# Performance work log

Hardware: AMD Instinct MI355X
Metric: run time of the kernel (lower is better)

The kernel has to match this reference:

```python
import jax, jax.numpy as jnp
import numpy as np

B, T, C, H = 4, 2048, 1024, 16
HD = C // H  # head dim = 64


def setup_inputs() -> dict:
    key = jax.random.key(0)
    k1, k2, k3, k4, k5 = jax.random.split(key, 5)
    s_in = 1.0 / np.sqrt(C)
    return {
        "x": jax.random.normal(k1, (B, T, C), dtype=jnp.float32),
        "W_attn": jax.random.uniform(k2, (C, 3 * C), dtype=jnp.float32, minval=-s_in, maxval=s_in),
        "b_attn": jax.random.uniform(k3, (3 * C,), dtype=jnp.float32, minval=-s_in, maxval=s_in),
        "W_proj": jax.random.uniform(k4, (C, C), dtype=jnp.float32, minval=-s_in, maxval=s_in),
        "b_proj": jax.random.uniform(k5, (C,), dtype=jnp.float32, minval=-s_in, maxval=s_in),
    }


def reference(x, W_attn, b_attn, W_proj, b_proj):
    Bx, Tx, Cx = x.shape
    qkv = x @ W_attn + b_attn                      # [B,T,3C]
    q, k, v = jnp.split(qkv, 3, axis=2)
    # [B,T,C] -> [B,H,T,HD]
    def heads(t):
        return t.reshape(Bx, Tx, H, HD).transpose(0, 2, 1, 3)
    q, k, v = heads(q), heads(k), heads(v)
    scale = 1.0 / np.sqrt(HD).astype(np.float32)
    att = jnp.einsum('bhqd,bhkd->bhqk', q, k) * scale
    causal = jnp.tril(jnp.ones((Tx, Tx), dtype=bool))
    att = jnp.where(causal[None, None], att, -jnp.inf)
    att = jax.nn.softmax(att, axis=-1)
    y = jnp.einsum('bhqk,bhkd->bhqd', att, v)      # [B,H,T,HD]
    y = y.transpose(0, 2, 1, 3).reshape(Bx, Tx, Cx)
    return y @ W_proj + b_proj
```

## Files before the change

### kernel.cpp

```cpp
#include <hip/hip_runtime.h>
#include <math.h>

#define Bn 4
#define Tn 2048
#define Cn 1024
#define Hn 16
#define HDn 64
#define Mn (Bn * Tn)

typedef unsigned short u16;
typedef unsigned int u32;
typedef __attribute__((ext_vector_type(8))) short bf16x8;
typedef __attribute__((ext_vector_type(8))) unsigned short us8;
typedef __attribute__((ext_vector_type(4))) float f32x4;
typedef __attribute__((ext_vector_type(16))) float f32x16;
typedef __attribute__((ext_vector_type(4))) unsigned int u32x4;

__device__ __forceinline__ float b2f(u16 u) {
    return __uint_as_float(((u32)u) << 16);
}
__device__ __forceinline__ u16 f2b(float f) {
    u32 u = __float_as_uint(f);
    return (u16)((u + 0x7FFFu + ((u >> 16) & 1u)) >> 16);
}
__device__ __forceinline__ u32 cvtpk(float a, float b) {
    u32 d;
    asm("v_cvt_pk_bf16_f32 %0, %1, %2" : "=v"(d) : "v"(a), "v"(b));
    return d;
}
__device__ __forceinline__ void pswap(u32& a, u32& b) {
    asm("v_permlane32_swap_b32 %0, %1" : "+v"(a), "+v"(b));
}

__device__ __forceinline__ int xcd_work(int bid, int nwg) {
    return (bid & 7) * (nwg >> 3) + (bid >> 3);
}

#define GLL(srcp, dstp)                                                     \
    __builtin_amdgcn_global_load_lds(                                       \
        (const __attribute__((address_space(1))) u32*)(srcp),               \
        (__attribute__((address_space(3))) u32*)(dstp), 16, 0, 0)

__global__ __launch_bounds__(256) void cvt_f32_bf16_kernel(
    const float4* __restrict__ in, ushort4* __restrict__ out, int n4)
{
    int i = blockIdx.x * 256 + threadIdx.x;
    if (i < n4) {
        float4 v = in[i];
        ushort4 o;
        o.x = f2b(v.x); o.y = f2b(v.y); o.z = f2b(v.z); o.w = f2b(v.w);
        out[i] = o;
    }
}

__global__ __launch_bounds__(256) void transpose_cvt_kernel(
    const float* __restrict__ in, u16* __restrict__ out, int R, int Cc)
{
    __shared__ u16 t[32][33];
    const int c0 = blockIdx.x * 32, r0 = blockIdx.y * 32;
    const int tx = threadIdx.x & 31, ty = threadIdx.x >> 5;
    #pragma unroll
    for (int i = 0; i < 32; i += 8)
        t[ty + i][tx] = f2b(in[(size_t)(r0 + ty + i) * Cc + c0 + tx]);
    __syncthreads();
    #pragma unroll
    for (int i = 0; i < 32; i += 8)
        out[(size_t)(c0 + ty + i) * R + r0 + tx] = t[tx][ty + i];
}

template <bool OUT_BF16, bool QKV_MODE>
__global__ __launch_bounds__(256) void gemm_bf16_kernel(
    const u16* __restrict__ A, const u16* __restrict__ BT,
    const float* __restrict__ bias,
    u16* __restrict__ outb, float* __restrict__ outf, u16* __restrict__ vTout,
    int N, int K, int nx)
{
    __shared__ u16 Al[128 * 32];
    __shared__ u16 Bl[128 * 32];

    const int tid = threadIdx.x;
    const int workid = xcd_work(blockIdx.x, gridDim.x);
    const int brow = (workid / nx) * 128;
    const int bcol = (workid % nx) * 128;
    const int w  = tid >> 6;
    const int wr = w >> 1, wc = w & 1;
    const int l  = tid & 63;
    const int lr = l & 15;
    const int lk = (l >> 4) << 3;

    f32x4 acc[4][4];
    #pragma unroll
    for (int m = 0; m < 4; ++m)
        #pragma unroll
        for (int n = 0; n < 4; ++n) acc[m][n] = (f32x4){0.f, 0.f, 0.f, 0.f};

    for (int k0 = 0; k0 < K; k0 += 32) {
        __syncthreads();
        #pragma unroll
        for (int i = 0; i < 2; ++i) {
            const int c   = i * 256 + tid;
            const int row = c >> 2;
            const int col = (c & 3) << 3;
            GLL(&A [(size_t)(brow + row) * K + k0 + col],
                &Al[(size_t)(i * 256 + (tid & 192)) * 8]);
            GLL(&BT[(size_t)(bcol + row) * K + k0 + col],
                &Bl[(size_t)(i * 256 + (tid & 192)) * 8]);
        }
        __syncthreads();

        bf16x8 a[4], b[4];
        #pragma unroll
        for (int m = 0; m < 4; ++m)
            a[m] = *(const bf16x8*)&Al[(wr * 64 + m * 16 + lr) * 32 + lk];
        #pragma unroll
        for (int n = 0; n < 4; ++n)
            b[n] = *(const bf16x8*)&Bl[(wc * 64 + n * 16 + lr) * 32 + lk];

        __builtin_amdgcn_s_setprio(1);
        #pragma unroll
        for (int m = 0; m < 4; ++m)
            #pragma unroll
            for (int n = 0; n < 4; ++n)
                acc[m][n] = __builtin_amdgcn_mfma_f32_16x16x32_bf16(
                    a[m], b[n], acc[m][n], 0, 0, 0);
        __builtin_amdgcn_s_setprio(0);
    }

    const int orow0 = brow + wr * 64 + ((l >> 4) << 2);
    const int ocol0 = bcol + wc * 64 + lr;
    if (QKV_MODE && bcol >= 2048) {
        #pragma unroll
        for (int n = 0; n < 4; ++n) {
            const int c = ocol0 + n * 16 - 2048;
            const float bv = bias[ocol0 + n * 16];
            #pragma unroll
            for (int m = 0; m < 4; ++m) {
                const int row0 = orow0 + m * 16;
                const int bb = row0 >> 11, t0 = row0 & 2047;
                ushort4 pk;
                pk.x = f2b(acc[m][n][0] + bv);
                pk.y = f2b(acc[m][n][1] + bv);
                pk.z = f2b(acc[m][n][2] + bv);
                pk.w = f2b(acc[m][n][3] + bv);
                *(ushort4*)&vTout[((size_t)bb * Cn + c) * Tn + t0] = pk;
            }
        }
    } else {
        #pragma unroll
        for (int n = 0; n < 4; ++n) {
            const int col = ocol0 + n * 16;
            const float bv = bias[col];
            #pragma unroll
            for (int m = 0; m < 4; ++m) {
                #pragma unroll
                for (int r = 0; r < 4; ++r) {
                    const int row = orow0 + m * 16 + r;
                    const float v = acc[m][n][r] + bv;
                    if (OUT_BF16) outb[(size_t)row * N + col] = f2b(v);
                    else          outf[(size_t)row * N + col] = v;
                }
            }
        }
    }
}

__global__ __launch_bounds__(256, 2) void attn_mfma6_kernel(
    const u16* __restrict__ qkvb, const u16* __restrict__ vT,
    u16* __restrict__ yb)
{
    __shared__ u16 Kb[2][64 * 64];
    __shared__ u16 Vb[2][64 * 64];

    const int tid = threadIdx.x;
    const int w   = tid >> 6;
    const int l   = tid & 63;
    const int q31 = l & 31;
    const int hi  = l >> 5;
    const int work = xcd_work(blockIdx.x, 512);
    const int pr  = work & 7;
    const int bh  = work >> 3;
    const int b   = bh >> 4, h = bh & 15;

    const float S2 = 0.18033688f;

    const u16* Kg = qkvb + (size_t)(b * Tn) * (3 * Cn) + Cn + h * HDn;
    const u16* Vg = vT + (size_t)bh * HDn * Tn;

    const int srow = l >> 3;
    const int schk = ((l & 7) ^ srow) << 3;
    const int rloc = w * 16;
    const int rsw8 = q31 & 7;

    #pragma unroll 1
    for (int half = 0; half < 2; ++half) {
        const int qt = half ? (15 - pr) : pr;
        const int ktmax = 2 * qt + 2;
        const int qrow0 = qt * 128 + w * 32;
        const int qglob = qrow0 + q31;

        const u16* Qp = qkvb + (size_t)(b * Tn + qglob) * (3 * Cn)
                        + h * HDn + hi * 8;
        bf16x8 qf[4];
        #pragma unroll
        for (int c = 0; c < 4; ++c) qf[c] = *(const bf16x8*)(Qp + c * 16);

        f32x16 O0, O1;
        #pragma unroll
        for (int r = 0; r < 16; ++r) { O0[r] = 0.f; O1[r] = 0.f; }
        float m = -INFINITY, ls = 0.f;

        #pragma unroll
        for (int jc = 0; jc < 2; ++jc) {
            const int rr = rloc + jc * 8;
            GLL(Kg + (size_t)(rr + srow) * (3 * Cn) + schk, &Kb[0][rr * 64]);
            GLL(Vg + (size_t)(rr + srow) * Tn + schk,       &Vb[0][rr * 64]);
        }
        __syncthreads();

        int cur = 0;
        for (int kt = 0; kt < ktmax; ++kt) {
            if (kt + 1 < ktmax) {
                #pragma unroll
                for (int jc = 0; jc < 2; ++jc) {
                    const int rr = rloc + jc * 8;
                    GLL(Kg + (size_t)((kt + 1) * 64 + rr + srow) * (3 * Cn) + schk,
                        &Kb[cur ^ 1][rr * 64]);
                    GLL(Vg + (size_t)(rr + srow) * Tn + (kt + 1) * 64 + schk,
                        &Vb[cur ^ 1][rr * 64]);
                }
            }
            const u16* Kc = Kb[cur];
            const u16* Vc = Vb[cur];

            if (kt * 64 <= qrow0 + 31) {
                f32x16 S0, S1;
                #pragma unroll
                for (int r = 0; r < 16; ++r) { S0[r] = 0.f; S1[r] = 0.f; }
                __builtin_amdgcn_s_setprio(1);
                #pragma unroll
                for (int c = 0; c < 4; ++c) {
                    const int co = ((2 * c + hi) ^ rsw8) << 3;
                    const bf16x8 k0 = *(const bf16x8*)&Kc[q31 * 64 + co];
                    const bf16x8 k1 = *(const bf16x8*)&Kc[(32 + q31) * 64 + co];
                    S0 = __builtin_amdgcn_mfma_f32_32x32x16_bf16(k0, qf[c], S0, 0, 0, 0);
                    S1 = __builtin_amdgcn_mfma_f32_32x32x16_bf16(k1, qf[c], S1, 0, 0, 0);
                }
                __builtin_amdgcn_s_setprio(0);

                if (kt * 64 + 63 > qrow0) {
                    #pragma unroll
                    for (int r = 0; r < 16; ++r) {
                        const int kl = kt * 64 + (r & 3) + 8 * (r >> 2) + 4 * hi;
                        if (kl > qglob)      S0[r] = -INFINITY;
                        if (kl + 32 > qglob) S1[r] = -INFINITY;
                    }
                }

                float mt = S0[0];
                #pragma unroll
                for (int r = 1; r < 16; ++r) mt = fmaxf(mt, S0[r]);
                #pragma unroll
                for (int r = 0; r < 16; ++r) mt = fmaxf(mt, S1[r]);
                mt = fmaxf(mt, __shfl_xor(mt, 32));

                float lscale = 1.f;
                if (__any(mt > m + 64.f)) {
                    const float mn = fmaxf(m, mt);
                    const float alpha = exp2f((m - mn) * S2);
                    m = mn; lscale = alpha;
                    #pragma unroll
                    for (int r = 0; r < 16; ++r) {
                        const int qloc = (r & 3) + 8 * (r >> 2) + 4 * hi;
                        const float ar = __shfl(alpha, qloc);
                        O0[r] *= ar; O1[r] *= ar;
                    }
                }

                float lt = 0.f;
                u32 w0[8], w1[8];
                #pragma unroll
                for (int i = 0; i < 8; ++i) {
                    const float p0 = exp2f((S0[2 * i]     - m) * S2);
                    const float p1 = exp2f((S0[2 * i + 1] - m) * S2);
                    const float p2 = exp2f((S1[2 * i]     - m) * S2);
                    const float p3 = exp2f((S1[2 * i + 1] - m) * S2);
                    lt += (p0 + p1) + (p2 + p3);
                    w0[i] = cvtpk(p0, p1);
                    w1[i] = cvtpk(p2, p3);
                }
                lt += __shfl_xor(lt, 32);
                ls = ls * lscale + lt;

                __builtin_amdgcn_s_setprio(1);
                #pragma unroll
                for (int t2 = 0; t2 < 2; ++t2) {
                    #pragma unroll
                    for (int c1 = 0; c1 < 2; ++c1) {
                        u32 a0 = t2 ? w1[4 * c1 + 0] : w0[4 * c1 + 0];
                        u32 b0 = t2 ? w1[4 * c1 + 2] : w0[4 * c1 + 2];
                        u32 a1 = t2 ? w1[4 * c1 + 1] : w0[4 * c1 + 1];
                        u32 b1 = t2 ? w1[4 * c1 + 3] : w0[4 * c1 + 3];
                        pswap(a0, b0);
                        pswap(a1, b1);
                        u32x4 fr; fr.x = a0; fr.y = a1; fr.z = b0; fr.w = b1;
                        const bf16x8 pf = __builtin_bit_cast(bf16x8, fr);
                        const int c = t2 * 2 + c1;
                        const int co = ((2 * c + hi) ^ rsw8) << 3;
                        const bf16x8 v0 = *(const bf16x8*)&Vc[q31 * 64 + co];
                        const bf16x8 v1 = *(const bf16x8*)&Vc[(32 + q31) * 64 + co];
                        O0 = __builtin_amdgcn_mfma_f32_32x32x16_bf16(pf, v0, O0, 0, 0, 0);
                        O1 = __builtin_amdgcn_mfma_f32_32x32x16_bf16(pf, v1, O1, 0, 0, 0);
                    }
                }
                __builtin_amdgcn_s_setprio(0);
            }

            __syncthreads();
            cur ^= 1;
        }

        #pragma unroll
        for (int r = 0; r < 16; ++r) {
            const int qloc = (r & 3) + 8 * (r >> 2) + 4 * hi;
            const float inv = __builtin_amdgcn_rcpf(__shfl(ls, qloc));
            u16* yp = yb + (size_t)(b * Tn + qrow0 + qloc) * Cn + h * HDn + q31;
            yp[0]  = f2b(O0[r] * inv);
            yp[32] = f2b(O1[r] * inv);
        }
    }
}

extern "C" void kernel_launch(void* const* d_in, const int* in_sizes, int n_in,
                              void* d_out, int out_size, void* d_ws, size_t ws_size,
                              hipStream_t stream)
{
    const float* x      = (const float*)d_in[0];
    const float* W_attn = (const float*)d_in[1];
    const float* b_attn = (const float*)d_in[2];
    const float* W_proj = (const float*)d_in[3];
    const float* b_proj = (const float*)d_in[4];
    float* out = (float*)d_out;

    u16* xb   = (u16*)d_ws;
    u16* WaT  = xb   + (size_t)Mn * Cn;
    u16* WpT  = WaT  + (size_t)3 * Cn * Cn;
    u16* qkvb = WpT  + (size_t)Cn * Cn;
    u16* yb   = qkvb + (size_t)Mn * 3 * Cn;
    u16* vT   = yb   + (size_t)Mn * Cn;

    cvt_f32_bf16_kernel<<<(Mn * Cn / 4 + 255) / 256, 256, 0, stream>>>(
        (const float4*)x, (ushort4*)xb, Mn * Cn / 4);

    transpose_cvt_kernel<<<dim3(3 * Cn / 32, Cn / 32), 256, 0, stream>>>(
        W_attn, WaT, Cn, 3 * Cn);
    transpose_cvt_kernel<<<dim3(Cn / 32, Cn / 32), 256, 0, stream>>>(
        W_proj, WpT, Cn, Cn);

    gemm_bf16_kernel<true, true><<<24 * 64, 256, 0, stream>>>(
        xb, WaT, b_attn, qkvb, nullptr, vT, 3 * Cn, Cn, 24);

    attn_mfma6_kernel<<<512, 256, 0, stream>>>(qkvb, vT, yb);

    gemm_bf16_kernel<false, false><<<8 * 64, 256, 0, stream>>>(
        yb, WpT, b_proj, nullptr, out, nullptr, Cn, Cn, 8);
}
```

Before: 202.4 us.

## Double-buffer GEMM LDS tiles and use grid-stride conversion kernel

```diff
diff --git a/kernel.cpp b/kernel.cpp
--- a/kernel.cpp
+++ b/kernel.cpp
@@ -44,8 +44,7 @@
 __global__ __launch_bounds__(256) void cvt_f32_bf16_kernel(
     const float4* __restrict__ in, ushort4* __restrict__ out, int n4)
 {
-    int i = blockIdx.x * 256 + threadIdx.x;
-    if (i < n4) {
+    for (int i = blockIdx.x * 256 + threadIdx.x; i < n4; i += gridDim.x * 256) {
         float4 v = in[i];
         ushort4 o;
         o.x = f2b(v.x); o.y = f2b(v.y); o.z = f2b(v.z); o.w = f2b(v.w);
@@ -75,8 +74,8 @@
     u16* __restrict__ outb, float* __restrict__ outf, u16* __restrict__ vTout,
     int N, int K, int nx)
 {
-    __shared__ u16 Al[128 * 32];
-    __shared__ u16 Bl[128 * 32];
+    __shared__ u16 Al[2][128 * 32];
+    __shared__ u16 Bl[2][128 * 32];
 
     const int tid = threadIdx.x;
     const int workid = xcd_work(blockIdx.x, gridDim.x);
@@ -88,33 +87,40 @@
     const int lr = l & 15;
     const int lk = (l >> 4) << 3;
 
+    const int r0s = tid >> 2,            c0s = (tid & 3) << 3;
+    const int r1s = (256 + tid) >> 2,    c1s = c0s;
+    const int d0s = (tid & 192) * 8;
+    const int d1s = (256 + (tid & 192)) * 8;
+
     f32x4 acc[4][4];
     #pragma unroll
     for (int m = 0; m < 4; ++m)
         #pragma unroll
         for (int n = 0; n < 4; ++n) acc[m][n] = (f32x4){0.f, 0.f, 0.f, 0.f};
 
+    GLL(&A [(size_t)(brow + r0s) * K + c0s], &Al[0][d0s]);
+    GLL(&BT[(size_t)(bcol + r0s) * K + c0s], &Bl[0][d0s]);
+    GLL(&A [(size_t)(brow + r1s) * K + c1s], &Al[0][d1s]);
+    GLL(&BT[(size_t)(bcol + r1s) * K + c1s], &Bl[0][d1s]);
+    __syncthreads();
+
+    int cur = 0;
     for (int k0 = 0; k0 < K; k0 += 32) {
-        __syncthreads();
-        #pragma unroll
-        for (int i = 0; i < 2; ++i) {
-            const int c   = i * 256 + tid;
-            const int row = c >> 2;
-            const int col = (c & 3) << 3;
-            GLL(&A [(size_t)(brow + row) * K + k0 + col],
-                &Al[(size_t)(i * 256 + (tid & 192)) * 8]);
-            GLL(&BT[(size_t)(bcol + row) * K + k0 + col],
-                &Bl[(size_t)(i * 256 + (tid & 192)) * 8]);
-        }
-        __syncthreads();
+        if (k0 + 32 < K) {
+            const int kn = k0 + 32;
+            GLL(&A [(size_t)(brow + r0s) * K + kn + c0s], &Al[cur ^ 1][d0s]);
+            GLL(&BT[(size_t)(bcol + r0s) * K + kn + c0s], &Bl[cur ^ 1][d0s]);
+            GLL(&A [(size_t)(brow + r1s) * K + kn + c1s], &Al[cur ^ 1][d1s]);
+            GLL(&BT[(size_t)(bcol + r1s) * K + kn + c1s], &Bl[cur ^ 1][d1s]);
+        }
 
         bf16x8 a[4], b[4];
         #pragma unroll
         for (int m = 0; m < 4; ++m)
-            a[m] = *(const bf16x8*)&Al[(wr * 64 + m * 16 + lr) * 32 + lk];
+            a[m] = *(const bf16x8*)&Al[cur][(wr * 64 + m * 16 + lr) * 32 + lk];
         #pragma unroll
         for (int n = 0; n < 4; ++n)
-            b[n] = *(const bf16x8*)&Bl[(wc * 64 + n * 16 + lr) * 32 + lk];
+            b[n] = *(const bf16x8*)&Bl[cur][(wc * 64 + n * 16 + lr) * 32 + lk];
 
         __builtin_amdgcn_s_setprio(1);
         #pragma unroll
@@ -124,6 +130,9 @@
                 acc[m][n] = __builtin_amdgcn_mfma_f32_16x16x32_bf16(
                     a[m], b[n], acc[m][n], 0, 0, 0);
         __builtin_amdgcn_s_setprio(0);
+
+        __syncthreads();
+        cur ^= 1;
     }
 
     const int orow0 = brow + wr * 64 + ((l >> 4) << 2);
@@ -348,7 +357,7 @@
     u16* yb   = qkvb + (size_t)Mn * 3 * Cn;
     u16* vT   = yb   + (size_t)Mn * Cn;
 
-    cvt_f32_bf16_kernel<<<(Mn * Cn / 4 + 255) / 256, 256, 0, stream>>>(
+    cvt_f32_bf16_kernel<<<2048, 256, 0, stream>>>(
         (const float4*)x, (ushort4*)xb, Mn * Cn / 4);
 
     transpose_cvt_kernel<<<dim3(3 * Cn / 32, Cn / 32), 256, 0, stream>>>(
```

Result: no change. 200.7 us (-0.9%).
